# Kernel optimization log

Hardware: AMD Instinct MI355X
Metric: run time of the kernel (lower is better)

## Reference

```python
import jax, jax.numpy as jnp
import numpy as np

EPS = 1e-5
GROUPS = 16
OUT_CH = 128
GC = OUT_CH // GROUPS  # group_channels = 8
SPAN = 128


def _bn(x, gamma, beta, axes):
    # BatchNorm in training mode: biased batch statistics over `axes`.
    m = jnp.mean(x, axis=axes, keepdims=True)
    v = jnp.var(x, axis=axes, keepdims=True)
    shape = [1] * x.ndim
    shape[1] = x.shape[1]
    g = gamma.reshape(shape)
    b = beta.reshape(shape)
    return (x - m) * jax.lax.rsqrt(v + EPS) * g + b


def setup_inputs() -> dict:
    key = jax.random.key(0)
    ks = jax.random.split(key, 3)
    x = jax.random.normal(ks[0], (2, 128, 64, 128), dtype=jnp.float32)
    W_qkv = jax.random.normal(ks[1], (2 * OUT_CH, 128), dtype=jnp.float32) * (1.0 / np.sqrt(128))
    rel_emb = jax.random.normal(ks[2], (2 * GC, 2 * SPAN - 1), dtype=jnp.float32)
    return {
        "x": x,
        "W_qkv": W_qkv,
        "gamma_qkv": jnp.ones((2 * OUT_CH,), jnp.float32),
        "beta_qkv": jnp.zeros((2 * OUT_CH,), jnp.float32),
        "rel_emb": rel_emb,
        "gamma_sim": jnp.ones((3 * GROUPS,), jnp.float32),
        "beta_sim": jnp.zeros((3 * GROUPS,), jnp.float32),
        "gamma_out": jnp.ones((2 * OUT_CH,), jnp.float32),
        "beta_out": jnp.zeros((2 * OUT_CH,), jnp.float32),
    }


def reference(x, W_qkv, gamma_qkv, beta_qkv, rel_emb, gamma_sim, beta_sim, gamma_out, beta_out):
    # dim == 1: attend over the width axis. x: [B, C, H, W], W == SPAN.
    B, C, H, W = x.shape
    xr = jnp.transpose(x, (0, 2, 1, 3)).reshape(B * H, C, W)  # [BH, C, W]

    # 1x1 Conv1d + BN1d -> query/key/value
    qkv = jnp.einsum('oc,bcl->bol', W_qkv, xr)  # [BH, 2*OUT, W]
    qkv = _bn(qkv, gamma_qkv, beta_qkv, axes=(0, 2))
    qkv = qkv.reshape(B * H, GROUPS, 2 * GC, W)
    q = qkv[:, :, : GC // 2]            # [BH, g, gc/2, W]
    k = qkv[:, :, GC // 2: GC]          # [BH, g, gc/2, W]
    v = qkv[:, :, GC:]                  # [BH, g, gc,   W]

    # relative position embeddings gathered into [2*gc, span, span]
    idx = jnp.arange(SPAN)[:, None] - jnp.arange(SPAN)[None, :] + SPAN - 1
    emb = rel_emb[:, idx]               # [2*gc, span, span]
    q_emb = emb[: GC // 2]
    k_emb = emb[GC // 2: GC]
    v_emb = emb[GC:]

    qe = jnp.einsum('bgci,cij->bgij', q, q_emb)   # [BH, g, W, W]
    ke = jnp.einsum('bgci,cij->bgij', k, k_emb)   # [BH, g, W, W]
    # faithful to original: contracts the first spatial axis of qe/ke
    qk = jnp.einsum('bgci,bgcj->bgij', qe, ke)    # [BH, g, W, W]

    sim = jnp.concatenate([qk, qe, ke], axis=1)   # [BH, 3g, W, W]
    sim = _bn(sim, gamma_sim, beta_sim, axes=(0, 2, 3))
    sim = sim.reshape(B * H, 3, GROUPS, W, W).sum(axis=1)  # [BH, g, W, W]
    sim = jax.nn.softmax(sim, axis=3)

    am = jnp.einsum('bgij,bgcj->bgci', sim, v)      # [BH, g, gc, W]
    ame = jnp.einsum('bgij,cij->bgci', sim, v_emb)  # [BH, g, gc, W]

    out = jnp.concatenate([am, ame], axis=-1).reshape(B * H, 2 * OUT_CH, W)
    out = _bn(out, gamma_out, beta_out, axes=(0, 2))
    out = out.reshape(B, H, OUT_CH, 2, W).sum(axis=-2)  # [B, H, OUT, W]
    return jnp.transpose(out, (0, 2, 1, 3))             # [B, OUT, H, W]
```

## Files before the change

kernel.cpp:

```cpp
#include <hip/hip_runtime.h>

#define EPS 1e-5f
typedef unsigned short u16;
typedef unsigned int u32;

typedef __attribute__((ext_vector_type(8))) short bf16x8;
typedef __attribute__((ext_vector_type(4))) float f32x4;

__device__ __forceinline__ float bf2f(u16 h) {
    u32 u = ((u32)h) << 16;
    return __builtin_bit_cast(float, u);
}
__device__ __forceinline__ u16 f2bf(float f) {
    u32 u = __builtin_bit_cast(u32, f);
    u32 r = (u + 0x7fffu + ((u >> 16) & 1u)) >> 16;
    return (u16)r;
}
__device__ __forceinline__ u32 pack2(float a, float b) {
    return (u32)f2bf(a) | ((u32)f2bf(b) << 16);
}
__device__ __forceinline__ float bflo(u32 u) {
    return __builtin_bit_cast(float, u << 16);
}
__device__ __forceinline__ float bfhi(u32 u) {
    return __builtin_bit_cast(float, u & 0xffff0000u);
}

__global__ __launch_bounds__(256) void k1_gemm_qkv(
    const float* __restrict__ x, const float* __restrict__ Wq,
    float* __restrict__ qkv, float* __restrict__ stats)
{
    __shared__ float Wt[64 * 68];
    __shared__ float xt[64 * 128];
    const int tid = threadIdx.x;
    const int ot = blockIdx.x;
    const int n  = blockIdx.y;
    const int b = n >> 6, h = n & 63;
    const int to = tid >> 5, tl = tid & 31;
    const int o0 = to * 8, l0 = tl * 4;

    float acc[8][4];
#pragma unroll
    for (int r = 0; r < 8; ++r) { acc[r][0]=0.f; acc[r][1]=0.f; acc[r][2]=0.f; acc[r][3]=0.f; }

    for (int cb = 0; cb < 128; cb += 64) {
        __syncthreads();
#pragma unroll
        for (int k = 0; k < 4; ++k) {
            int f = tid + k * 256;
            int oo = f >> 4, c4 = f & 15;
            float4 v = *(const float4*)(Wq + (ot * 64 + oo) * 128 + cb + c4 * 4);
            *(float4*)(Wt + oo * 68 + c4 * 4) = v;
        }
#pragma unroll
        for (int k = 0; k < 8; ++k) {
            int f = tid + k * 256;
            int c = f >> 5, l4 = f & 31;
            float4 v = *(const float4*)(x + ((size_t)((b * 128 + cb + c) * 64 + h)) * 128 + l4 * 4);
            *(float4*)(xt + c * 128 + l4 * 4) = v;
        }
        __syncthreads();
#pragma unroll 4
        for (int c = 0; c < 64; ++c) {
            float4 xv = *(const float4*)(xt + c * 128 + l0);
#pragma unroll
            for (int r = 0; r < 8; ++r) {
                float w = Wt[(o0 + r) * 68 + c];
                acc[r][0] += w * xv.x; acc[r][1] += w * xv.y;
                acc[r][2] += w * xv.z; acc[r][3] += w * xv.w;
            }
        }
    }

#pragma unroll
    for (int r = 0; r < 8; ++r) {
        int o = ot * 64 + o0 + r;
        *(float4*)(qkv + ((size_t)n * 256 + o) * 128 + l0) =
            make_float4(acc[r][0], acc[r][1], acc[r][2], acc[r][3]);
        float s  = acc[r][0] + acc[r][1] + acc[r][2] + acc[r][3];
        float sq = acc[r][0]*acc[r][0] + acc[r][1]*acc[r][1] + acc[r][2]*acc[r][2] + acc[r][3]*acc[r][3];
#pragma unroll
        for (int m = 1; m < 32; m <<= 1) {
            s  += __shfl_xor(s, m);
            sq += __shfl_xor(sq, m);
        }
        if (tl == 0) {
            atomicAdd(&stats[o], s);
            atomicAdd(&stats[256 + o], sq);
        }
    }
}

__global__ void k3_coef_qkv(const float* __restrict__ stats,
                            const float* __restrict__ gamma, const float* __restrict__ beta,
                            float* __restrict__ coef)
{
    int o = threadIdx.x;
    const float cnt = 16384.f;
    float mean = stats[o] / cnt;
    float var  = stats[256 + o] / cnt - mean * mean;
    float a = gamma[o] * rsqrtf(var + EPS);
    coef[o] = a;
    coef[256 + o] = beta[o] - a * mean;
}

__global__ __launch_bounds__(512, 4) void k4_pass1(
    const float* __restrict__ qkv, const float* __restrict__ rel,
    const float* __restrict__ cq, u16* __restrict__ qk,
    float* __restrict__ stats)
{
    __shared__ u16 QEb[128 * 136];
    __shared__ u16 KEb[128 * 136];
    __shared__ float red[8 * 6];
    const int tid = threadIdx.x;
    const int n = blockIdx.x >> 4, g = blockIdx.x & 15;

    const int pt = tid & 31, pi = tid >> 5;
    const int t0 = pt * 4, i0 = pi * 8;
    const int d0 = t0 - i0 + 120;

    float qes = 0.f, qesq = 0.f, kes = 0.f, kesq = 0.f;

#pragma unroll
    for (int mat = 0; mat < 2; ++mat) {
        float qv[4][4];
#pragma unroll
        for (int c = 0; c < 4; ++c) {
            int o = g * 16 + mat * 4 + c;
            float a = cq[o], bb = cq[256 + o];
            float4 x0 = *(const float4*)(qkv + ((size_t)n * 256 + o) * 128 + t0);
            qv[c][0] = fmaf(a, x0.x, bb); qv[c][1] = fmaf(a, x0.y, bb);
            qv[c][2] = fmaf(a, x0.z, bb); qv[c][3] = fmaf(a, x0.w, bb);
        }
        float rr[4][12];
#pragma unroll
        for (int c = 0; c < 4; ++c) {
            const float* p = rel + (mat * 4 + c) * 255 + d0;
#pragma unroll
            for (int j = 0; j < 3; ++j) {
                float4 v = *(const float4*)(p + j * 4);
                rr[c][j*4+0] = v.x; rr[c][j*4+1] = v.y;
                rr[c][j*4+2] = v.z; rr[c][j*4+3] = v.w;
            }
        }
        u16* MB = mat ? KEb : QEb;
        float s = 0.f, sq = 0.f;
#pragma unroll
        for (int ii = 0; ii < 8; ++ii) {
            float vv[4];
#pragma unroll
            for (int tt = 0; tt < 4; ++tt) {
                int dl = tt - ii + 7;
                float v = qv[0][tt] * rr[0][dl] + qv[1][tt] * rr[1][dl]
                        + qv[2][tt] * rr[2][dl] + qv[3][tt] * rr[3][dl];
                vv[tt] = v;
                s += v; sq = fmaf(v, v, sq);
            }
            *(uint2*)(MB + (i0 + ii) * 136 + t0) =
                make_uint2(pack2(vv[0], vv[1]), pack2(vv[2], vv[3]));
        }
        if (mat == 0) { qes = s; qesq = sq; } else { kes = s; kesq = sq; }
    }
    __syncthreads();

    const int lane = tid & 63, wv = tid >> 6;
    const int fm = lane & 15, fq = lane >> 4;

    f32x4 acc[8];
#pragma unroll
    for (int tj = 0; tj < 8; ++tj) acc[tj] = (f32x4){0.f, 0.f, 0.f, 0.f};

#pragma unroll
    for (int kb = 0; kb < 4; ++kb) {
        const int ko = kb * 32 + fq * 8;
        bf16x8 a0 = *(const bf16x8*)(QEb + (wv * 16 + fm) * 136 + ko);
#pragma unroll
        for (int tj = 0; tj < 8; ++tj) {
            bf16x8 bfr = *(const bf16x8*)(KEb + (tj * 16 + fm) * 136 + ko);
            acc[tj] = __builtin_amdgcn_mfma_f32_16x16x32_bf16(a0, bfr, acc[tj], 0, 0, 0);
        }
    }

    float qks = 0.f, qksq = 0.f;
#pragma unroll
    for (int tj = 0; tj < 8; ++tj) {
#pragma unroll
        for (int r = 0; r < 4; ++r) {
            float v = acc[tj][r];
            qks += v; qksq = fmaf(v, v, qksq);
            QEb[(wv * 16 + fq * 4 + r) * 136 + tj * 16 + fm] = f2bf(v);
        }
    }

#pragma unroll
    for (int m = 1; m < 64; m <<= 1) {
        qes += __shfl_xor(qes, m);  qesq += __shfl_xor(qesq, m);
        kes += __shfl_xor(kes, m);  kesq += __shfl_xor(kesq, m);
        qks += __shfl_xor(qks, m);  qksq += __shfl_xor(qksq, m);
    }
    if (lane == 0) {
        red[wv * 6 + 0] = qes; red[wv * 6 + 1] = qesq;
        red[wv * 6 + 2] = kes; red[wv * 6 + 3] = kesq;
        red[wv * 6 + 4] = qks; red[wv * 6 + 5] = qksq;
    }
    __syncthreads();

    u16* qkg = qk + (size_t)(n * 16 + g) * 16384;
#pragma unroll
    for (int k = 0; k < 4; ++k) {
        int f = tid + k * 512;
        int row = f >> 4, c8 = f & 15;
        uint4 v = *(const uint4*)(QEb + row * 136 + c8 * 8);
        *(uint4*)(qkg + ((c8 >> 1) * 128 + row) * 16 + (c8 & 1) * 8) = v;
    }

    if (tid < 6) {
        float tot = 0.f;
#pragma unroll
        for (int w = 0; w < 8; ++w) tot += red[w * 6 + tid];
        int off = (tid & 1) ? 560 : 512;
        int ch = (tid < 2) ? (16 + g) : (tid < 4) ? (32 + g) : g;
        atomicAdd(&stats[off + ch], tot);
    }
}

__global__ void k5_coef_sim(const float* __restrict__ stats,
                            const float* __restrict__ gamma, const float* __restrict__ beta,
                            float* __restrict__ coef)
{
    int ch = threadIdx.x;
    if (ch < 48) {
        const float cnt = 2097152.f;
        float mean = stats[512 + ch] / cnt;
        float var  = stats[560 + ch] / cnt - mean * mean;
        float a = gamma[ch] * rsqrtf(var + EPS);
        coef[ch] = a;
        coef[48 + ch] = beta[ch] - a * mean;
    }
}

#define K6_STEP(rb, rv, vv, qkf)                                             \
    {                                                                        \
        float qe = q0 * bf2f((u16)rb[0]) + q1 * bf2f((u16)rb[1])             \
                 + q2 * bf2f((u16)rb[2]) + q3 * bf2f((u16)rb[3]);            \
        float ke = k0 * bf2f((u16)rb[4]) + k1 * bf2f((u16)rb[5])             \
                 + k2 * bf2f((u16)rb[6]) + k3 * bf2f((u16)rb[7]);            \
        float s = fmaf(aqk, (qkf), qe + ke + bsum);                          \
        float e = __expf(s);                                                 \
        l += e;                                                              \
        _Pragma("unroll")                                                    \
        for (int c = 0; c < 8; ++c) {                                        \
            am[c]  = fmaf(e, bf2f((u16)vv[c]), am[c]);                       \
            ame[c] = fmaf(e, bf2f((u16)rv[c]), ame[c]);                      \
        }                                                                    \
    }

#define K6_JS(ddv, jjv, w0, w1)                                              \
    {                                                                        \
        const int dd = (ddv); const int jj = (jjv);                          \
        bf16x8 rb0 = *(const bf16x8*)(relb + (dd    ) * 24);                 \
        bf16x8 rb1 = *(const bf16x8*)(relb + (dd - 1) * 24);                 \
        bf16x8 rb2 = *(const bf16x8*)(relb + (dd - 2) * 24);                 \
        bf16x8 rb3 = *(const bf16x8*)(relb + (dd - 3) * 24);                 \
        bf16x8 rv0 = *(const bf16x8*)(relb + (dd    ) * 24 + 8);             \
        bf16x8 rv1 = *(const bf16x8*)(relb + (dd - 1) * 24 + 8);             \
        bf16x8 rv2 = *(const bf16x8*)(relb + (dd - 2) * 24 + 8);             \
        bf16x8 rv3 = *(const bf16x8*)(relb + (dd - 3) * 24 + 8);             \
        bf16x8 vv0 = *(const bf16x8*)(vb + (jj + 0) * 8);                    \
        bf16x8 vv1 = *(const bf16x8*)(vb + (jj + 1) * 8);                    \
        bf16x8 vv2 = *(const bf16x8*)(vb + (jj + 2) * 8);                    \
        bf16x8 vv3 = *(const bf16x8*)(vb + (jj + 3) * 8);                    \
        K6_STEP(rb0, rv0, vv0, bflo(w0));                                    \
        K6_STEP(rb1, rv1, vv1, bfhi(w0));                                    \
        K6_STEP(rb2, rv2, vv2, bflo(w1));                                    \
        K6_STEP(rb3, rv3, vv3, bfhi(w1));                                    \
    }

__global__ __launch_bounds__(128, 4) void k6_pass2(
    const float* __restrict__ qkv, const float* __restrict__ rel,
    const float* __restrict__ cq, const float* __restrict__ cs,
    const u16* __restrict__ qk,
    float* __restrict__ outraw, float* __restrict__ ostats)
{
    __shared__ u16 relb[256 * 24];
    __shared__ u16 vb[128 * 8];
    __shared__ float qn_s[8 * 128];
    const int tid = threadIdx.x;
    const int n = blockIdx.x >> 4, g = blockIdx.x & 15;

#pragma unroll
    for (int k = 0; k < 32; ++k) {
        int f = tid + k * 128;
        int c = f >> 8, d = f & 255;
        if (d < 255) relb[d * 24 + c] = f2bf(rel[c * 255 + d]);
    }
#pragma unroll
    for (int k = 0; k < 8; ++k) {
        int f = tid + k * 128;
        int c = f >> 7, t = f & 127;
        int o = g * 16 + c;
        qn_s[f] = fmaf(cq[o], qkv[((size_t)n * 256 + o) * 128 + t], cq[256 + o]);
    }
#pragma unroll
    for (int k = 0; k < 8; ++k) {
        int f = tid + k * 128;
        int c = f >> 7, j = f & 127;
        int o = g * 16 + 8 + c;
        float v = fmaf(cq[o], qkv[((size_t)n * 256 + o) * 128 + j], cq[256 + o]);
        vb[j * 8 + c] = f2bf(v);
    }
    __syncthreads();

    const float aqk = cs[g], aqe = cs[16 + g], ake = cs[32 + g];
    const float bsum = cs[48 + g] + cs[64 + g] + cs[80 + g];
    const int i = tid;

    const u16* qkg = qk + (size_t)(n * 16 + g) * 16384 + i * 16;

    uint4 qA = *(const uint4*)(qkg);
    uint4 qB = *(const uint4*)(qkg + 8);

    float q0 = aqe * qn_s[i],       q1 = aqe * qn_s[128 + i];
    float q2 = aqe * qn_s[256 + i], q3 = aqe * qn_s[384 + i];
    float k0 = ake * qn_s[512 + i], k1 = ake * qn_s[640 + i];
    float k2 = ake * qn_s[768 + i], k3 = ake * qn_s[896 + i];

    float l = 0.f;
    float am[8], ame[8];
#pragma unroll
    for (int c = 0; c < 8; ++c) { am[c] = 0.f; ame[c] = 0.f; }

#pragma unroll
    for (int jc = 0; jc < 8; ++jc) {
        uint4 nA, nB;
        if (jc < 7) {
            nA = *(const uint4*)(qkg + (jc + 1) * 2048);
            nB = *(const uint4*)(qkg + (jc + 1) * 2048 + 8);
        }

        const int dbase = i + 127 - jc * 16;
        K6_JS(dbase,      jc * 16,      qA.x, qA.y);
        K6_JS(dbase - 4,  jc * 16 + 4,  qA.z, qA.w);
        K6_JS(dbase - 8,  jc * 16 + 8,  qB.x, qB.y);
        K6_JS(dbase - 12, jc * 16 + 12, qB.z, qB.w);

        if (jc < 7) { qA = nA; qB = nB; }
    }

    float inv = 1.f / l;
    float o16[16];
#pragma unroll
    for (int c = 0; c < 8; ++c) { o16[2 * c] = am[c] * inv; o16[2 * c + 1] = ame[c] * inv; }

    float* orow = outraw + ((size_t)n * 256 + g * 16) * 128 + i;
#pragma unroll
    for (int c16 = 0; c16 < 16; ++c16) orow[c16 * 128] = o16[c16];

    const int lane = tid & 63;
#pragma unroll
    for (int c16 = 0; c16 < 16; ++c16) {
        float sv = o16[c16], sq = o16[c16] * o16[c16];
#pragma unroll
        for (int mm = 1; mm < 64; mm <<= 1) { sv += __shfl_xor(sv, mm); sq += __shfl_xor(sq, mm); }
        if (lane == 0) {
            atomicAdd(&ostats[g * 16 + c16], sv);
            atomicAdd(&ostats[256 + g * 16 + c16], sq);
        }
    }
}

__global__ void k7_coef_out(const float* __restrict__ stats,
                            const float* __restrict__ gamma, const float* __restrict__ beta,
                            float* __restrict__ coef)
{
    int o = threadIdx.x;
    const float cnt = 16384.f;
    float mean = stats[608 + o] / cnt;
    float var  = stats[864 + o] / cnt - mean * mean;
    float a = gamma[o] * rsqrtf(var + EPS);
    coef[o] = a;
    coef[256 + o] = beta[o] - a * mean;
}

__global__ __launch_bounds__(256) void k8_final(
    const float* __restrict__ outraw, const float* __restrict__ co,
    float* __restrict__ out)
{
    int idx = blockIdx.x * 256 + threadIdx.x;
    int w  = idx & 127;
    int h  = (idx >> 7) & 63;
    int oc = (idx >> 13) & 127;
    int b  = idx >> 20;
    int n  = b * 64 + h;
    int o0 = oc * 2;
    float x0 = outraw[((size_t)n * 256 + o0) * 128 + w];
    float x1 = outraw[((size_t)n * 256 + o0 + 1) * 128 + w];
    out[idx] = (co[o0] * x0 + co[256 + o0]) + (co[o0 + 1] * x1 + co[256 + o0 + 1]);
}

extern "C" void kernel_launch(void* const* d_in, const int* in_sizes, int n_in,
                              void* d_out, int out_size, void* d_ws, size_t ws_size,
                              hipStream_t stream)
{
    const float* x   = (const float*)d_in[0];
    const float* Wq  = (const float*)d_in[1];
    const float* gq  = (const float*)d_in[2];
    const float* bq  = (const float*)d_in[3];
    const float* rel = (const float*)d_in[4];
    const float* gs  = (const float*)d_in[5];
    const float* bs  = (const float*)d_in[6];
    const float* go  = (const float*)d_in[7];
    const float* bo  = (const float*)d_in[8];

    float* ws     = (float*)d_ws;
    float* qkv    = ws;
    float* outraw = ws + 4194304;
    u16*   qk     = (u16*)(ws + 8388608);
    float* stats  = ws + 25165824;
    float* cq     = stats + 1120;
    float* cs     = stats + 1632;
    float* co     = stats + 1728;

    (void)hipMemsetAsync(stats, 0, 1120 * sizeof(float), stream);

    k1_gemm_qkv<<<dim3(4, 128), 256, 0, stream>>>(x, Wq, qkv, stats);
    k3_coef_qkv<<<1, 256, 0, stream>>>(stats, gq, bq, cq);
    k4_pass1<<<2048, 512, 0, stream>>>(qkv, rel, cq, qk, stats);
    k5_coef_sim<<<1, 64, 0, stream>>>(stats, gs, bs, cs);
    k6_pass2<<<2048, 128, 0, stream>>>(qkv, rel, cq, cs, qk, outraw, stats + 608);
    k7_coef_out<<<1, 256, 0, stream>>>(stats, go, bo, co);
    k8_final<<<8192, 256, 0, stream>>>(outraw, co, (float*)d_out);
}
```

Before: 333.7 us.

## Split pass2 key range across two thread halves and merge via shared memory

The attention pass2 kernel now runs 256 threads per block. Each half of the block handles half of the key columns for the same query row, and the partial softmax sums and accumulators are combined through shared memory, which reuses the relb buffer. This doubles the parallelism per block and cuts the serial loop length per thread, at the cost of an extra reduction step and two more barriers. The constant bias sum is also dropped from the exponent, since a shift that is the same for every key cancels in the softmax. Without max subtraction, this also removes a term that could affect overflow range.

```diff
diff --git a/kernel.cpp b/kernel.cpp
--- a/kernel.cpp
+++ b/kernel.cpp
@@ -245,7 +245,7 @@
                  + q2 * bf2f((u16)rb[2]) + q3 * bf2f((u16)rb[3]);            \
         float ke = k0 * bf2f((u16)rb[4]) + k1 * bf2f((u16)rb[5])             \
                  + k2 * bf2f((u16)rb[6]) + k3 * bf2f((u16)rb[7]);            \
-        float s = fmaf(aqk, (qkf), qe + ke + bsum);                          \
+        float s = fmaf(aqk, (qkf), qe + ke);                                 \
         float e = __expf(s);                                                 \
         l += e;                                                              \
         _Pragma("unroll")                                                    \
@@ -276,7 +276,7 @@
         K6_STEP(rb3, rv3, vv3, bfhi(w1));                                    \
     }
 
-__global__ __launch_bounds__(128, 4) void k6_pass2(
+__global__ __launch_bounds__(256, 4) void k6_pass2(
     const float* __restrict__ qkv, const float* __restrict__ rel,
     const float* __restrict__ cq, const float* __restrict__ cs,
     const u16* __restrict__ qk,
@@ -289,21 +289,21 @@
     const int n = blockIdx.x >> 4, g = blockIdx.x & 15;
 
 #pragma unroll
-    for (int k = 0; k < 32; ++k) {
-        int f = tid + k * 128;
+    for (int k = 0; k < 16; ++k) {
+        int f = tid + k * 256;
         int c = f >> 8, d = f & 255;
         if (d < 255) relb[d * 24 + c] = f2bf(rel[c * 255 + d]);
     }
 #pragma unroll
-    for (int k = 0; k < 8; ++k) {
-        int f = tid + k * 128;
+    for (int k = 0; k < 4; ++k) {
+        int f = tid + k * 256;
         int c = f >> 7, t = f & 127;
         int o = g * 16 + c;
         qn_s[f] = fmaf(cq[o], qkv[((size_t)n * 256 + o) * 128 + t], cq[256 + o]);
     }
 #pragma unroll
-    for (int k = 0; k < 8; ++k) {
-        int f = tid + k * 128;
+    for (int k = 0; k < 4; ++k) {
+        int f = tid + k * 256;
         int c = f >> 7, j = f & 127;
         int o = g * 16 + 8 + c;
         float v = fmaf(cq[o], qkv[((size_t)n * 256 + o) * 128 + j], cq[256 + o]);
@@ -312,13 +312,12 @@
     __syncthreads();
 
     const float aqk = cs[g], aqe = cs[16 + g], ake = cs[32 + g];
-    const float bsum = cs[48 + g] + cs[64 + g] + cs[80 + g];
-    const int i = tid;
+    const int i = tid & 127, hf = tid >> 7;
 
     const u16* qkg = qk + (size_t)(n * 16 + g) * 16384 + i * 16;
 
-    uint4 qA = *(const uint4*)(qkg);
-    uint4 qB = *(const uint4*)(qkg + 8);
+    uint4 qA = *(const uint4*)(qkg + (size_t)(hf * 4) * 2048);
+    uint4 qB = *(const uint4*)(qkg + (size_t)(hf * 4) * 2048 + 8);
 
     float q0 = aqe * qn_s[i],       q1 = aqe * qn_s[128 + i];
     float q2 = aqe * qn_s[256 + i], q3 = aqe * qn_s[384 + i];
@@ -331,40 +330,58 @@
     for (int c = 0; c < 8; ++c) { am[c] = 0.f; ame[c] = 0.f; }
 
 #pragma unroll
-    for (int jc = 0; jc < 8; ++jc) {
+    for (int jq = 0; jq < 4; ++jq) {
+        const int jc = hf * 4 + jq;
         uint4 nA, nB;
-        if (jc < 7) {
-            nA = *(const uint4*)(qkg + (jc + 1) * 2048);
-            nB = *(const uint4*)(qkg + (jc + 1) * 2048 + 8);
+        if (jq < 3) {
+            nA = *(const uint4*)(qkg + (size_t)(jc + 1) * 2048);
+            nB = *(const uint4*)(qkg + (size_t)(jc + 1) * 2048 + 8);
         }
 
         const int dbase = i + 127 - jc * 16;
-        K6_JS(dbase,      jc * 16,      qA.x, qA.y);
-        K6_JS(dbase - 4,  jc * 16 + 4,  qA.z, qA.w);
-        K6_JS(dbase - 8,  jc * 16 + 8,  qB.x, qB.y);
-        K6_JS(dbase - 12, jc * 16 + 12, qB.z, qB.w);
-
-        if (jc < 7) { qA = nA; qB = nB; }
-    }
-
-    float inv = 1.f / l;
-    float o16[16];
-#pragma unroll
-    for (int c = 0; c < 8; ++c) { o16[2 * c] = am[c] * inv; o16[2 * c + 1] = ame[c] * inv; }
-
-    float* orow = outraw + ((size_t)n * 256 + g * 16) * 128 + i;
-#pragma unroll
-    for (int c16 = 0; c16 < 16; ++c16) orow[c16 * 128] = o16[c16];
-
-    const int lane = tid & 63;
-#pragma unroll
-    for (int c16 = 0; c16 < 16; ++c16) {
-        float sv = o16[c16], sq = o16[c16] * o16[c16];
-#pragma unroll
-        for (int mm = 1; mm < 64; mm <<= 1) { sv += __shfl_xor(sv, mm); sq += __shfl_xor(sq, mm); }
-        if (lane == 0) {
-            atomicAdd(&ostats[g * 16 + c16], sv);
-            atomicAdd(&ostats[256 + g * 16 + c16], sq);
+        const int jb = jc * 16;
+        K6_JS(dbase,      jb,      qA.x, qA.y);
+        K6_JS(dbase - 4,  jb + 4,  qA.z, qA.w);
+        K6_JS(dbase - 8,  jb + 8,  qB.x, qB.y);
+        K6_JS(dbase - 12, jb + 12, qB.z, qB.w);
+
+        if (jq < 3) { qA = nA; qB = nB; }
+    }
+
+    __syncthreads();
+    float* red = (float*)relb;
+    if (hf) {
+        float* r = red + i * 17;
+#pragma unroll
+        for (int c = 0; c < 8; ++c) { r[c] = am[c]; r[8 + c] = ame[c]; }
+        r[16] = l;
+    }
+    __syncthreads();
+    if (!hf) {
+        const float* r = red + i * 17;
+#pragma unroll
+        for (int c = 0; c < 8; ++c) { am[c] += r[c]; ame[c] += r[8 + c]; }
+        l += r[16];
+
+        float inv = 1.f / l;
+        float o16[16];
+#pragma unroll
+        for (int c = 0; c < 8; ++c) { o16[2 * c] = am[c] * inv; o16[2 * c + 1] = ame[c] * inv; }
+
+        float* orow = outraw + ((size_t)n * 256 + g * 16) * 128 + i;
+#pragma unroll
+        for (int c16 = 0; c16 < 16; ++c16) orow[c16 * 128] = o16[c16];
+
+        const int lane = tid & 63;
+#pragma unroll
+        for (int c16 = 0; c16 < 16; ++c16) {
+            float sv = o16[c16], sq = o16[c16] * o16[c16];
+#pragma unroll
+            for (int mm = 1; mm < 64; mm <<= 1) { sv += __shfl_xor(sv, mm); sq += __shfl_xor(sq, mm); }
+            if (lane == 0) {
+                atomicAdd(&ostats[g * 16 + c16], sv);
+                atomicAdd(&ostats[256 + g * 16 + c16], sq);
+            }
         }
     }
 }
@@ -427,7 +444,7 @@
     k3_coef_qkv<<<1, 256, 0, stream>>>(stats, gq, bq, cq);
     k4_pass1<<<2048, 512, 0, stream>>>(qkv, rel, cq, qk, stats);
     k5_coef_sim<<<1, 64, 0, stream>>>(stats, gs, bs, cs);
-    k6_pass2<<<2048, 128, 0, stream>>>(qkv, rel, cq, cs, qk, outraw, stats + 608);
+    k6_pass2<<<2048, 256, 0, stream>>>(qkv, rel, cq, cs, qk, outraw, stats + 608);
     k7_coef_out<<<1, 256, 0, stream>>>(stats, go, bo, co);
     k8_final<<<8192, 256, 0, stream>>>(outraw, co, (float*)d_out);
 }
```

Measured after the change: 1.311 ms. 293% more time.

## Split pass2 blocks across value-channel halves and shrink shared-memory footprint

Applied to the files above, without the earlier changes.

The attention pass-2 kernel now launches twice as many blocks, and each block handles half of the value channels: 4 of the am and 4 of the ame outputs instead of 8 each. Shared memory is split into a packed q/k embedding table plus smaller per-half value tables, and the q/k row values are read straight from global into registers instead of being staged in LDS. Launch bounds are raised so more blocks fit per CU, and the per-row softmax bias sum is dropped because it cancels in the normalization. The cost is that each half recomputes the full qe/ke/exp work and reloads the qk tile, duplicating that part of the computation.

```diff
diff --git a/kernel.cpp b/kernel.cpp
--- a/kernel.cpp
+++ b/kernel.cpp
@@ -5,6 +5,7 @@
 typedef unsigned int u32;
 
 typedef __attribute__((ext_vector_type(8))) short bf16x8;
+typedef __attribute__((ext_vector_type(4))) short bf16x4;
 typedef __attribute__((ext_vector_type(4))) float f32x4;
 
 __device__ __forceinline__ float bf2f(u16 h) {
@@ -245,126 +246,135 @@
                  + q2 * bf2f((u16)rb[2]) + q3 * bf2f((u16)rb[3]);            \
         float ke = k0 * bf2f((u16)rb[4]) + k1 * bf2f((u16)rb[5])             \
                  + k2 * bf2f((u16)rb[6]) + k3 * bf2f((u16)rb[7]);            \
-        float s = fmaf(aqk, (qkf), qe + ke + bsum);                          \
+        float s = fmaf(aqk, (qkf), qe + ke);                                 \
         float e = __expf(s);                                                 \
         l += e;                                                              \
-        _Pragma("unroll")                                                    \
-        for (int c = 0; c < 8; ++c) {                                        \
-            am[c]  = fmaf(e, bf2f((u16)vv[c]), am[c]);                       \
-            ame[c] = fmaf(e, bf2f((u16)rv[c]), ame[c]);                      \
-        }                                                                    \
+        am[0] = fmaf(e, bf2f((u16)vv[0]), am[0]);                            \
+        am[1] = fmaf(e, bf2f((u16)vv[1]), am[1]);                            \
+        am[2] = fmaf(e, bf2f((u16)vv[2]), am[2]);                            \
+        am[3] = fmaf(e, bf2f((u16)vv[3]), am[3]);                            \
+        ame[0] = fmaf(e, bf2f((u16)rv[0]), ame[0]);                          \
+        ame[1] = fmaf(e, bf2f((u16)rv[1]), ame[1]);                          \
+        ame[2] = fmaf(e, bf2f((u16)rv[2]), ame[2]);                          \
+        ame[3] = fmaf(e, bf2f((u16)rv[3]), ame[3]);                          \
     }
 
 #define K6_JS(ddv, jjv, w0, w1)                                              \
     {                                                                        \
         const int dd = (ddv); const int jj = (jjv);                          \
-        bf16x8 rb0 = *(const bf16x8*)(relb + (dd    ) * 24);                 \
-        bf16x8 rb1 = *(const bf16x8*)(relb + (dd - 1) * 24);                 \
-        bf16x8 rb2 = *(const bf16x8*)(relb + (dd - 2) * 24);                 \
-        bf16x8 rb3 = *(const bf16x8*)(relb + (dd - 3) * 24);                 \
-        bf16x8 rv0 = *(const bf16x8*)(relb + (dd    ) * 24 + 8);             \
-        bf16x8 rv1 = *(const bf16x8*)(relb + (dd - 1) * 24 + 8);             \
-        bf16x8 rv2 = *(const bf16x8*)(relb + (dd - 2) * 24 + 8);             \
-        bf16x8 rv3 = *(const bf16x8*)(relb + (dd - 3) * 24 + 8);             \
-        bf16x8 vv0 = *(const bf16x8*)(vb + (jj + 0) * 8);                    \
-        bf16x8 vv1 = *(const bf16x8*)(vb + (jj + 1) * 8);                    \
-        bf16x8 vv2 = *(const bf16x8*)(vb + (jj + 2) * 8);                    \
-        bf16x8 vv3 = *(const bf16x8*)(vb + (jj + 3) * 8);                    \
+        bf16x8 rb0 = *(const bf16x8*)(rbq + (dd    ) * 8);                   \
+        bf16x8 rb1 = *(const bf16x8*)(rbq + (dd - 1) * 8);                   \
+        bf16x8 rb2 = *(const bf16x8*)(rbq + (dd - 2) * 8);                   \
+        bf16x8 rb3 = *(const bf16x8*)(rbq + (dd - 3) * 8);                   \
+        bf16x4 rv0 = *(const bf16x4*)(rvb + (dd    ) * 4);                   \
+        bf16x4 rv1 = *(const bf16x4*)(rvb + (dd - 1) * 4);                   \
+        bf16x4 rv2 = *(const bf16x4*)(rvb + (dd - 2) * 4);                   \
+        bf16x4 rv3 = *(const bf16x4*)(rvb + (dd - 3) * 4);                   \
+        bf16x4 vv0 = *(const bf16x4*)(vb + (jj + 0) * 4);                    \
+        bf16x4 vv1 = *(const bf16x4*)(vb + (jj + 1) * 4);                    \
+        bf16x4 vv2 = *(const bf16x4*)(vb + (jj + 2) * 4);                    \
+        bf16x4 vv3 = *(const bf16x4*)(vb + (jj + 3) * 4);                    \
         K6_STEP(rb0, rv0, vv0, bflo(w0));                                    \
         K6_STEP(rb1, rv1, vv1, bfhi(w0));                                    \
         K6_STEP(rb2, rv2, vv2, bflo(w1));                                    \
         K6_STEP(rb3, rv3, vv3, bfhi(w1));                                    \
     }
 
-__global__ __launch_bounds__(128, 4) void k6_pass2(
+__global__ __launch_bounds__(128, 6) void k6_pass2(
     const float* __restrict__ qkv, const float* __restrict__ rel,
     const float* __restrict__ cq, const float* __restrict__ cs,
     const u16* __restrict__ qk,
     float* __restrict__ outraw, float* __restrict__ ostats)
 {
-    __shared__ u16 relb[256 * 24];
-    __shared__ u16 vb[128 * 8];
-    __shared__ float qn_s[8 * 128];
+    __shared__ __align__(16) u16 rbq[255 * 8];
+    __shared__ __align__(16) u16 rvb[255 * 4];
+    __shared__ __align__(16) u16 vb[128 * 4];
     const int tid = threadIdx.x;
-    const int n = blockIdx.x >> 4, g = blockIdx.x & 15;
-
-#pragma unroll
-    for (int k = 0; k < 32; ++k) {
+    const int bid = blockIdx.x;
+    const int half = bid & 1, g = (bid >> 1) & 15, n = bid >> 5;
+
+#pragma unroll
+    for (int k = 0; k < 16; ++k) {
         int f = tid + k * 128;
         int c = f >> 8, d = f & 255;
-        if (d < 255) relb[d * 24 + c] = f2bf(rel[c * 255 + d]);
+        if (d < 255) rbq[d * 8 + c] = f2bf(rel[c * 255 + d]);
     }
 #pragma unroll
     for (int k = 0; k < 8; ++k) {
         int f = tid + k * 128;
-        int c = f >> 7, t = f & 127;
-        int o = g * 16 + c;
-        qn_s[f] = fmaf(cq[o], qkv[((size_t)n * 256 + o) * 128 + t], cq[256 + o]);
-    }
-#pragma unroll
-    for (int k = 0; k < 8; ++k) {
+        int c = f >> 8, d = f & 255;
+        if (d < 255) rvb[d * 4 + c] = f2bf(rel[(8 + half * 4 + c) * 255 + d]);
+    }
+#pragma unroll
+    for (int k = 0; k < 4; ++k) {
         int f = tid + k * 128;
         int c = f >> 7, j = f & 127;
-        int o = g * 16 + 8 + c;
+        int o = g * 16 + 8 + half * 4 + c;
         float v = fmaf(cq[o], qkv[((size_t)n * 256 + o) * 128 + j], cq[256 + o]);
-        vb[j * 8 + c] = f2bf(v);
-    }
-    __syncthreads();
+        vb[j * 4 + c] = f2bf(v);
+    }
 
     const float aqk = cs[g], aqe = cs[16 + g], ake = cs[32 + g];
-    const float bsum = cs[48 + g] + cs[64 + g] + cs[80 + g];
     const int i = tid;
+
+    const float* qb = qkv + ((size_t)n * 256 + g * 16) * 128 + i;
+    float q0 = aqe * fmaf(cq[g*16+0], qb[0*128], cq[256+g*16+0]);
+    float q1 = aqe * fmaf(cq[g*16+1], qb[1*128], cq[256+g*16+1]);
+    float q2 = aqe * fmaf(cq[g*16+2], qb[2*128], cq[256+g*16+2]);
+    float q3 = aqe * fmaf(cq[g*16+3], qb[3*128], cq[256+g*16+3]);
+    float k0 = ake * fmaf(cq[g*16+4], qb[4*128], cq[256+g*16+4]);
+    float k1 = ake * fmaf(cq[g*16+5], qb[5*128], cq[256+g*16+5]);
+    float k2 = ake * fmaf(cq[g*16+6], qb[6*128], cq[256+g*16+6]);
+    float k3 = ake * fmaf(cq[g*16+7], qb[7*128], cq[256+g*16+7]);
 
     const u16* qkg = qk + (size_t)(n * 16 + g) * 16384 + i * 16;
 
     uint4 qA = *(const uint4*)(qkg);
     uint4 qB = *(const uint4*)(qkg + 8);
 
-    float q0 = aqe * qn_s[i],       q1 = aqe * qn_s[128 + i];
-    float q2 = aqe * qn_s[256 + i], q3 = aqe * qn_s[384 + i];
-    float k0 = ake * qn_s[512 + i], k1 = ake * qn_s[640 + i];
-    float k2 = ake * qn_s[768 + i], k3 = ake * qn_s[896 + i];
+    __syncthreads();
 
     float l = 0.f;
-    float am[8], ame[8];
-#pragma unroll
-    for (int c = 0; c < 8; ++c) { am[c] = 0.f; ame[c] = 0.f; }
+    float am[4], ame[4];
+#pragma unroll
+    for (int c = 0; c < 4; ++c) { am[c] = 0.f; ame[c] = 0.f; }
 
 #pragma unroll
     for (int jc = 0; jc < 8; ++jc) {
         uint4 nA, nB;
         if (jc < 7) {
-            nA = *(const uint4*)(qkg + (jc + 1) * 2048);
-            nB = *(const uint4*)(qkg + (jc + 1) * 2048 + 8);
+            nA = *(const uint4*)(qkg + (size_t)(jc + 1) * 2048);
+            nB = *(const uint4*)(qkg + (size_t)(jc + 1) * 2048 + 8);
         }
 
         const int dbase = i + 127 - jc * 16;
-        K6_JS(dbase,      jc * 16,      qA.x, qA.y);
-        K6_JS(dbase - 4,  jc * 16 + 4,  qA.z, qA.w);
-        K6_JS(dbase - 8,  jc * 16 + 8,  qB.x, qB.y);
-        K6_JS(dbase - 12, jc * 16 + 12, qB.z, qB.w);
+        const int jb = jc * 16;
+        K6_JS(dbase,      jb,      qA.x, qA.y);
+        K6_JS(dbase - 4,  jb + 4,  qA.z, qA.w);
+        K6_JS(dbase - 8,  jb + 8,  qB.x, qB.y);
+        K6_JS(dbase - 12, jb + 12, qB.z, qB.w);
 
         if (jc < 7) { qA = nA; qB = nB; }
     }
 
     float inv = 1.f / l;
-    float o16[16];
-#pragma unroll
-    for (int c = 0; c < 8; ++c) { o16[2 * c] = am[c] * inv; o16[2 * c + 1] = ame[c] * inv; }
-
-    float* orow = outraw + ((size_t)n * 256 + g * 16) * 128 + i;
-#pragma unroll
-    for (int c16 = 0; c16 < 16; ++c16) orow[c16 * 128] = o16[c16];
+    float o8[8];
+#pragma unroll
+    for (int c = 0; c < 4; ++c) { o8[2 * c] = am[c] * inv; o8[2 * c + 1] = ame[c] * inv; }
+
+    float* orow = outraw + ((size_t)n * 256 + g * 16 + half * 8) * 128 + i;
+#pragma unroll
+    for (int c8 = 0; c8 < 8; ++c8) orow[c8 * 128] = o8[c8];
 
     const int lane = tid & 63;
 #pragma unroll
-    for (int c16 = 0; c16 < 16; ++c16) {
-        float sv = o16[c16], sq = o16[c16] * o16[c16];
+    for (int c8 = 0; c8 < 8; ++c8) {
+        float sv = o8[c8], sq = o8[c8] * o8[c8];
 #pragma unroll
         for (int mm = 1; mm < 64; mm <<= 1) { sv += __shfl_xor(sv, mm); sq += __shfl_xor(sq, mm); }
         if (lane == 0) {
-            atomicAdd(&ostats[g * 16 + c16], sv);
-            atomicAdd(&ostats[256 + g * 16 + c16], sq);
+            atomicAdd(&ostats[g * 16 + half * 8 + c8], sv);
+            atomicAdd(&ostats[256 + g * 16 + half * 8 + c8], sq);
         }
     }
 }
@@ -427,7 +437,7 @@
     k3_coef_qkv<<<1, 256, 0, stream>>>(stats, gq, bq, cq);
     k4_pass1<<<2048, 512, 0, stream>>>(qkv, rel, cq, qk, stats);
     k5_coef_sim<<<1, 64, 0, stream>>>(stats, gs, bs, cs);
-    k6_pass2<<<2048, 128, 0, stream>>>(qkv, rel, cq, cs, qk, outraw, stats + 608);
+    k6_pass2<<<4096, 128, 0, stream>>>(qkv, rel, cq, cs, qk, outraw, stats + 608);
     k7_coef_out<<<1, 256, 0, stream>>>(stats, go, bo, co);
     k8_final<<<8192, 256, 0, stream>>>(outraw, co, (float*)d_out);
 }
```

Result: faster. 326.2 us (-2.3%).
